# Performance work log

Hardware: AMD Instinct MI355X
Metric: run time of the kernel (lower is better)

Reference implementation:

```python
import jax, jax.numpy as jnp
import numpy as np

HIDDEN = 2048
N_HEADS = 32
N_KV_HEADS = 8
HEAD_DIM = HIDDEN // N_HEADS  # 64
KV_DIM = N_KV_HEADS * HEAD_DIM  # 512


def setup_inputs() -> dict:
    key = jax.random.key(0)
    ks = jax.random.split(key, 9)
    s = 1.0 / np.sqrt(HIDDEN)
    x = jax.random.normal(ks[0], (2, 2048, HIDDEN), dtype=jnp.float32)
    wq = jax.random.uniform(ks[1], (HIDDEN, HIDDEN), jnp.float32, -s, s)
    bq = jax.random.uniform(ks[2], (HIDDEN,), jnp.float32, -s, s)
    wk = jax.random.uniform(ks[3], (KV_DIM, HIDDEN), jnp.float32, -s, s)
    bk = jax.random.uniform(ks[4], (KV_DIM,), jnp.float32, -s, s)
    wv = jax.random.uniform(ks[5], (KV_DIM, HIDDEN), jnp.float32, -s, s)
    bv = jax.random.uniform(ks[6], (KV_DIM,), jnp.float32, -s, s)
    wo = jax.random.uniform(ks[7], (HIDDEN, HIDDEN), jnp.float32, -s, s)
    bo = jax.random.uniform(ks[8], (HIDDEN,), jnp.float32, -s, s)
    return {"x": x, "wq": wq, "bq": bq, "wk": wk, "bk": bk,
            "wv": wv, "bv": bv, "wo": wo, "bo": bo}


def reference(x, wq, bq, wk, bk, wv, bv, wo, bo):
    B, S, _ = x.shape
    group = N_HEADS // N_KV_HEADS  # 4
    # projections (torch Linear: x @ W.T + b)
    q = (x @ wq.T + bq).reshape(B, S, N_HEADS, HEAD_DIM).transpose(0, 2, 1, 3)      # [B,H,S,D]
    k = (x @ wk.T + bk).reshape(B, S, N_KV_HEADS, HEAD_DIM).transpose(0, 2, 1, 3)   # [B,Hk,S,D]
    v = (x @ wv.T + bv).reshape(B, S, N_KV_HEADS, HEAD_DIM).transpose(0, 2, 1, 3)
    # repeat_interleave KV heads to match query heads
    k = jnp.repeat(k, group, axis=1)  # [B,H,S,D]
    v = jnp.repeat(v, group, axis=1)
    scale = 1.0 / np.sqrt(HEAD_DIM).astype(np.float32)
    attn = jnp.einsum('bhqd,bhkd->bhqk', q, k) * scale  # [B,H,S,S]
    score = jax.nn.softmax(attn, axis=-1)
    out = jnp.einsum('bhqk,bhkd->bhqd', score, v)       # [B,H,S,D]
    out = out.transpose(0, 2, 1, 3).reshape(B, S, HIDDEN)
    return out @ wo.T + bo
```

## Files before the change

kernel.cpp:

```cpp
#include <hip/hip_runtime.h>

typedef __attribute__((ext_vector_type(8))) short bf16x8;
typedef __attribute__((ext_vector_type(4))) float f32x4;
typedef __attribute__((ext_vector_type(16))) float f32x16;

__device__ __forceinline__ short f2b(float f) {
  union { unsigned u; float f; } c;
  c.f = f;
  unsigned r = (c.u + 0x7FFFu + ((c.u >> 16) & 1u)) >> 16;
  return (short)r;
}

__device__ __forceinline__ int cvt_pk_bf16(float lo, float hi) {
  int r;
  asm("v_cvt_pk_bf16_f32 %0, %1, %2" : "=v"(r) : "v"(lo), "v"(hi));
  return r;
}

__device__ __forceinline__ void plswap(int& a, int& b) {
  asm volatile("v_permlane32_swap_b32 %0, %1" : "+v"(a), "+v"(b));
}

__device__ __forceinline__ void async16(const void* g, void* l) {
  __builtin_amdgcn_global_load_lds(
      (const __attribute__((address_space(1))) unsigned*)g,
      (__attribute__((address_space(3))) unsigned*)l, 16, 0, 0);
}

__global__ __launch_bounds__(256)
void f32_to_bf16(const float* __restrict__ src, short* __restrict__ dst, int n) {
  int i = (blockIdx.x * blockDim.x + threadIdx.x) * 4;
  if (i < n) {
    float4 v = *(const float4*)(src + i);
    short4 o;
    o.x = f2b(v.x); o.y = f2b(v.y); o.z = f2b(v.z); o.w = f2b(v.w);
    *(short4*)(dst + i) = o;
  }
}

template <bool F32OUT>
__global__ __launch_bounds__(256)
void gemm_bt_bias(const short* __restrict__ A, const short* __restrict__ Bw,
                  const float* __restrict__ bias, void* __restrict__ Cv,
                  int M, int N, int K) {
  __shared__ short lsA[128 * 32];
  __shared__ short lsB[128 * 32];
  const int tid  = threadIdx.x;
  const int wave = tid >> 6, lane = tid & 63;
  const int quad = lane >> 4, lrow = lane & 15;
  const int m0 = blockIdx.y * 128, n0 = blockIdx.x * 128;
  const int wm = (wave >> 1) * 64, wn = (wave & 1) * 64;

  f32x4 zero = {0.f, 0.f, 0.f, 0.f};
  f32x4 acc[4][4];
#pragma unroll
  for (int i = 0; i < 4; i++)
#pragma unroll
    for (int j = 0; j < 4; j++) acc[i][j] = zero;

  const int r0 = tid >> 2, c0 = (tid & 3) * 8;
  const short* Ab  = A  + (size_t)(m0 + r0) * K + c0;
  const short* Ab2 = A  + (size_t)(m0 + r0 + 64) * K + c0;
  const short* Bb  = Bw + (size_t)(n0 + r0) * K + c0;
  const short* Bb2 = Bw + (size_t)(n0 + r0 + 64) * K + c0;

  for (int k0 = 0; k0 < K; k0 += 32) {
    async16(Ab  + k0, lsA + tid * 8);
    async16(Ab2 + k0, lsA + (tid + 256) * 8);
    async16(Bb  + k0, lsB + tid * 8);
    async16(Bb2 + k0, lsB + (tid + 256) * 8);
    __syncthreads();

    bf16x8 af[4], bfr[4];
#pragma unroll
    for (int i = 0; i < 4; i++)
      af[i] = *(const bf16x8*)(lsA + (wm + i * 16 + lrow) * 32 + quad * 8);
#pragma unroll
    for (int j = 0; j < 4; j++)
      bfr[j] = *(const bf16x8*)(lsB + (wn + j * 16 + lrow) * 32 + quad * 8);
#pragma unroll
    for (int i = 0; i < 4; i++)
#pragma unroll
      for (int j = 0; j < 4; j++)
        acc[i][j] = __builtin_amdgcn_mfma_f32_16x16x32_bf16(af[i], bfr[j], acc[i][j], 0, 0, 0);
    __syncthreads();
  }

#pragma unroll
  for (int j = 0; j < 4; j++) {
    const int col = n0 + wn + j * 16 + lrow;
    const float bv = bias[col];
#pragma unroll
    for (int i = 0; i < 4; i++) {
      const int rowb = m0 + wm + i * 16 + quad * 4;
#pragma unroll
      for (int r = 0; r < 4; r++) {
        const float val = acc[i][j][r] + bv;
        if (F32OUT)
          ((float*)Cv)[(size_t)(rowb + r) * N + col] = val;
        else
          ((short*)Cv)[(size_t)(rowb + r) * N + col] = f2b(val);
      }
    }
  }
}

__global__ __launch_bounds__(256)
void gemm_qkv(const short* __restrict__ A, const short* __restrict__ Bw,
              const float* __restrict__ bq, const float* __restrict__ bk,
              const float* __restrict__ bv,
              short* __restrict__ Qo, short* __restrict__ Ko, short* __restrict__ Vo) {
  const int K = 2048;
  __shared__ short lsA[128 * 32];
  __shared__ short lsB[128 * 32];
  const int tid  = threadIdx.x;
  const int wave = tid >> 6, lane = tid & 63;
  const int quad = lane >> 4, lrow = lane & 15;
  const int m0 = blockIdx.y * 128, n0 = blockIdx.x * 128;
  const int wm = (wave >> 1) * 64, wn = (wave & 1) * 64;

  f32x4 zero = {0.f, 0.f, 0.f, 0.f};
  f32x4 acc[4][4];
#pragma unroll
  for (int i = 0; i < 4; i++)
#pragma unroll
    for (int j = 0; j < 4; j++) acc[i][j] = zero;

  const int r0 = tid >> 2, c0 = (tid & 3) * 8;
  const short* Ab  = A  + (size_t)(m0 + r0) * K + c0;
  const short* Ab2 = A  + (size_t)(m0 + r0 + 64) * K + c0;
  const short* Bb  = Bw + (size_t)(n0 + r0) * K + c0;
  const short* Bb2 = Bw + (size_t)(n0 + r0 + 64) * K + c0;

  for (int k0 = 0; k0 < K; k0 += 32) {
    async16(Ab  + k0, lsA + tid * 8);
    async16(Ab2 + k0, lsA + (tid + 256) * 8);
    async16(Bb  + k0, lsB + tid * 8);
    async16(Bb2 + k0, lsB + (tid + 256) * 8);
    __syncthreads();

    bf16x8 af[4], bfr[4];
#pragma unroll
    for (int i = 0; i < 4; i++)
      af[i] = *(const bf16x8*)(lsA + (wm + i * 16 + lrow) * 32 + quad * 8);
#pragma unroll
    for (int j = 0; j < 4; j++)
      bfr[j] = *(const bf16x8*)(lsB + (wn + j * 16 + lrow) * 32 + quad * 8);
#pragma unroll
    for (int i = 0; i < 4; i++)
#pragma unroll
      for (int j = 0; j < 4; j++)
        acc[i][j] = __builtin_amdgcn_mfma_f32_16x16x32_bf16(af[i], bfr[j], acc[i][j], 0, 0, 0);
    __syncthreads();
  }

  short* base; int stride, coff; const float* bias;
  if (n0 < 2048)      { base = Qo; stride = 2048; bias = bq; coff = 0; }
  else if (n0 < 2560) { base = Ko; stride = 512;  bias = bk; coff = 2048; }
  else                { base = Vo; stride = 512;  bias = bv; coff = 2560; }
  const float qs = (n0 < 2048) ? 0.18033688011112043f : 1.0f;

#pragma unroll
  for (int j = 0; j < 4; j++) {
    const int lc = n0 + wn + j * 16 + lrow - coff;
    const float bvv = bias[lc];
#pragma unroll
    for (int i = 0; i < 4; i++) {
      const int rowb = m0 + wm + i * 16 + quad * 4;
#pragma unroll
      for (int r = 0; r < 4; r++)
        base[(size_t)(rowb + r) * stride + lc] = f2b((acc[i][j][r] + bvv) * qs);
    }
  }
}

#define S_LEN 2048
#define HID   2048
#define KVD   512
#define ST    72

__global__ __launch_bounds__(256)
void gqa_flash(const short* __restrict__ Q, const short* __restrict__ Kb,
               const short* __restrict__ Vb, short* __restrict__ O) {
  __shared__ __align__(16) short lsK[64 * ST];
  __shared__ __align__(16) short lsVt[64 * ST];
  __shared__ float lsum[4][32];

  const int tid  = threadIdx.x;
  const int wave = tid >> 6, lane = tid & 63;
  const int l31  = lane & 31, hl = lane >> 5;

  const int d  = blockIdx.x + (blockIdx.y << 6);
  const int by = ((d & 7) << 1) | (d >> 9);
  const int qb = (d >> 3) & 63;
  const int b = by >> 3, kvh = by & 7;
  const int h = kvh * 4 + wave;
  const int q0 = qb * 32;

  const short* Qrow = Q + (size_t)(b * S_LEN + q0 + l31) * HID + h * 64 + hl * 8;
  bf16x8 qf[4];
#pragma unroll
  for (int f = 0; f < 4; f++) qf[f] = *(const bf16x8*)(Qrow + f * 16);

  f32x16 o0, o1;
#pragma unroll
  for (int i = 0; i < 16; i++) { o0[i] = 0.f; o1[i] = 0.f; }
  float lloc = 0.f;

  const short* Kp = Kb + (size_t)b * S_LEN * KVD + kvh * 64;
  const short* Vp = Vb + (size_t)b * S_LEN * KVD + kvh * 64;

  const int keyA = tid >> 3, chK = (tid & 7) * 8;
  const int kpV = tid & 31, dcV = (tid >> 5) * 8;

  bf16x8 kf0 = *(const bf16x8*)(Kp + (size_t)keyA * KVD + chK);
  bf16x8 kf1 = *(const bf16x8*)(Kp + (size_t)(keyA + 32) * KVD + chK);
  bf16x8 vf0 = *(const bf16x8*)(Vp + (size_t)(2 * kpV) * KVD + dcV);
  bf16x8 vf1 = *(const bf16x8*)(Vp + (size_t)(2 * kpV + 1) * KVD + dcV);

  for (int k0 = 0; k0 < S_LEN; k0 += 64) {
    *(bf16x8*)(lsK + keyA * ST + chK) = kf0;
    *(bf16x8*)(lsK + (keyA + 32) * ST + chK) = kf1;
#pragma unroll
    for (int jj = 0; jj < 8; jj++) {
      unsigned pk = (unsigned)(unsigned short)vf0[jj] |
                    ((unsigned)(unsigned short)vf1[jj] << 16);
      *(unsigned*)(lsVt + (dcV + jj) * ST + 2 * kpV) = pk;
    }
    __syncthreads();

    const int kn = (k0 + 64) & (S_LEN - 1);
    kf0 = *(const bf16x8*)(Kp + (size_t)(kn + keyA) * KVD + chK);
    kf1 = *(const bf16x8*)(Kp + (size_t)(kn + keyA + 32) * KVD + chK);
    vf0 = *(const bf16x8*)(Vp + (size_t)(kn + 2 * kpV) * KVD + dcV);
    vf1 = *(const bf16x8*)(Vp + (size_t)(kn + 2 * kpV + 1) * KVD + dcV);

    f32x16 s0, s1;
#pragma unroll
    for (int i = 0; i < 16; i++) { s0[i] = 0.f; s1[i] = 0.f; }
    __builtin_amdgcn_s_setprio(1);
#pragma unroll
    for (int f = 0; f < 4; f++) {
      bf16x8 ka = *(const bf16x8*)(lsK + l31 * ST + f * 16 + hl * 8);
      bf16x8 kb = *(const bf16x8*)(lsK + (32 + l31) * ST + f * 16 + hl * 8);
      s0 = __builtin_amdgcn_mfma_f32_32x32x16_bf16(ka, qf[f], s0, 0, 0, 0);
      s1 = __builtin_amdgcn_mfma_f32_32x32x16_bf16(kb, qf[f], s1, 0, 0, 0);
    }
    __builtin_amdgcn_s_setprio(0);

#pragma unroll
    for (int i = 0; i < 16; i++) {
      s0[i] = __builtin_amdgcn_exp2f(s0[i]);
      s1[i] = __builtin_amdgcn_exp2f(s1[i]);
    }
    {
      f32x16 ps = s0 + s1;
      float a0 = (ps[0] + ps[1]) + (ps[2] + ps[3]);
      float a1 = (ps[4] + ps[5]) + (ps[6] + ps[7]);
      float a2 = (ps[8] + ps[9]) + (ps[10] + ps[11]);
      float a3 = (ps[12] + ps[13]) + (ps[14] + ps[15]);
      lloc += (a0 + a1) + (a2 + a3);
    }
    int P2[2][8];
#pragma unroll
    for (int qq = 0; qq < 8; qq++) {
      P2[0][qq] = cvt_pk_bf16(s0[2 * qq], s0[2 * qq + 1]);
      P2[1][qq] = cvt_pk_bf16(s1[2 * qq], s1[2 * qq + 1]);
    }

    __builtin_amdgcn_s_setprio(1);
#pragma unroll
    for (int t = 0; t < 4; t++) {
      const int j = t >> 1, b0 = (t & 1) * 4;
      int w0 = P2[j][b0 + 0], w2 = P2[j][b0 + 2];
      int w1 = P2[j][b0 + 1], w3 = P2[j][b0 + 3];
      plswap(w0, w2);
      plswap(w1, w3);
      union { unsigned u[4]; bf16x8 v; } pa;
      pa.u[0] = (unsigned)w0; pa.u[1] = (unsigned)w1;
      pa.u[2] = (unsigned)w2; pa.u[3] = (unsigned)w3;
      bf16x8 bv0 = *(const bf16x8*)(lsVt + l31 * ST + t * 16 + hl * 8);
      bf16x8 bv1 = *(const bf16x8*)(lsVt + (32 + l31) * ST + t * 16 + hl * 8);
      o0 = __builtin_amdgcn_mfma_f32_32x32x16_bf16(pa.v, bv0, o0, 0, 0, 0);
      o1 = __builtin_amdgcn_mfma_f32_32x32x16_bf16(pa.v, bv1, o1, 0, 0, 0);
    }
    __builtin_amdgcn_s_setprio(0);
    __syncthreads();
  }

  const float lfull = lloc + __shfl(lloc, lane ^ 32);
  if (lane < 32) lsum[wave][lane] = lfull;
#pragma unroll
  for (int r = 0; r < 16; r++) {
    const int qrow = (r & 3) + 8 * (r >> 2) + 4 * hl;
    const float rl = 1.0f / lsum[wave][qrow];
    short* op = O + (size_t)(b * S_LEN + q0 + qrow) * HID + h * 64 + l31;
    op[0]  = f2b(o0[r] * rl);
    op[32] = f2b(o1[r] * rl);
  }
}

extern "C" void kernel_launch(void* const* d_in, const int* in_sizes, int n_in,
                              void* d_out, int out_size, void* d_ws, size_t ws_size,
                              hipStream_t stream) {
  const float* x  = (const float*)d_in[0];
  const float* wq = (const float*)d_in[1];
  const float* bq = (const float*)d_in[2];
  const float* wk = (const float*)d_in[3];
  const float* bk = (const float*)d_in[4];
  const float* wv = (const float*)d_in[5];
  const float* bv = (const float*)d_in[6];
  const float* wo = (const float*)d_in[7];
  const float* bo = (const float*)d_in[8];
  float* out = (float*)d_out;

  short* xb  = (short*)d_ws;
  short* wqb = xb  + (size_t)4096 * 2048;
  short* wkb = wqb + (size_t)2048 * 2048;
  short* wvb = wkb + (size_t)512 * 2048;
  short* wob = wvb + (size_t)512 * 2048;
  short* Qb  = wob + (size_t)2048 * 2048;
  short* Kb  = Qb  + (size_t)4096 * 2048;
  short* Vb  = Kb  + (size_t)4096 * 512;
  short* AO  = Vb  + (size_t)4096 * 512;

  dim3 blk(256);
  f32_to_bf16<<<4096 * 2048 / 1024, blk, 0, stream>>>(x,  xb,  4096 * 2048);
  f32_to_bf16<<<2048 * 2048 / 1024, blk, 0, stream>>>(wq, wqb, 2048 * 2048);
  f32_to_bf16<<< 512 * 2048 / 1024, blk, 0, stream>>>(wk, wkb, 512 * 2048);
  f32_to_bf16<<< 512 * 2048 / 1024, blk, 0, stream>>>(wv, wvb, 512 * 2048);
  f32_to_bf16<<<2048 * 2048 / 1024, blk, 0, stream>>>(wo, wob, 2048 * 2048);

  gemm_qkv<<<dim3(3072 / 128, 4096 / 128), blk, 0, stream>>>(xb, wqb, bq, bk, bv, Qb, Kb, Vb);
  gqa_flash<<<dim3(2048 / 32, 16), blk, 0, stream>>>(Qb, Kb, Vb, AO);
  gemm_bt_bias<true><<<dim3(2048 / 128, 4096 / 128), blk, 0, stream>>>(AO, wob, bo, out, 4096, 2048, 2048);
}
```

Baseline: 334.6 us.

## Replace projection GEMMs with 256x256 double-buffered pipelined swizzled LDS kernel

Both projection GEMMs (fused QKV and output) now use a single templated kernel with 256x256 tiles, 512 threads, and K-step 64. It double-buffers LDS with async global-to-LDS loads interleaved between MFMA quarter-blocks, and uses XOR-swizzled LDS addressing to avoid bank conflicts. It also remaps workgroup IDs for cache locality and raises MFMA wave priority. The aim is to hide memory latency and raise data reuse per tile. The cost is heavy LDS use (128KB per block) and fewer blocks, which could hurt occupancy or tail behaviour on the smaller output GEMM grid.

```diff
diff --git a/kernel.cpp b/kernel.cpp
--- a/kernel.cpp
+++ b/kernel.cpp
@@ -38,138 +38,184 @@
   }
 }
 
-template <bool F32OUT>
-__global__ __launch_bounds__(256)
-void gemm_bt_bias(const short* __restrict__ A, const short* __restrict__ Bw,
-                  const float* __restrict__ bias, void* __restrict__ Cv,
-                  int M, int N, int K) {
-  __shared__ short lsA[128 * 32];
-  __shared__ short lsB[128 * 32];
+#define GBAR()  do { __builtin_amdgcn_s_barrier(); \
+                     __builtin_amdgcn_sched_barrier(0); } while (0)
+#define WAITV6() do { asm volatile("s_waitcnt vmcnt(6)" ::: "memory"); \
+                      __builtin_amdgcn_sched_barrier(0); } while (0)
+#define WAITV0() do { asm volatile("s_waitcnt vmcnt(0)" ::: "memory"); \
+                      __builtin_amdgcn_sched_barrier(0); } while (0)
+
+template <int MODE>
+__global__ __launch_bounds__(512, 2)
+void gemm256(const short* __restrict__ A, const short* __restrict__ Bw,
+             const float* __restrict__ bq, const float* __restrict__ bk,
+             const float* __restrict__ bv, float* __restrict__ Cf,
+             short* __restrict__ Qo, short* __restrict__ Ko,
+             short* __restrict__ Vo) {
+  constexpr int K  = 2048;
+  constexpr int NT = K / 64;
+  __shared__ short lsA[2][256 * 64];
+  __shared__ short lsB[2][256 * 64];
+
   const int tid  = threadIdx.x;
-  const int wave = tid >> 6, lane = tid & 63;
+  const int lane = tid & 63, wid = tid >> 6;
   const int quad = lane >> 4, lrow = lane & 15;
-  const int m0 = blockIdx.y * 128, n0 = blockIdx.x * 128;
-  const int wm = (wave >> 1) * 64, wn = (wave & 1) * 64;
-
+  const int wr = wid >> 2, wc = wid & 3;
+
+  const int GX  = gridDim.x;
+  const int nwg = GX * gridDim.y;
+  const int dd  = blockIdx.x + blockIdx.y * GX;
+  const int logical = (dd & 7) * (nwg >> 3) + (dd >> 3);
+  const int m0 = (logical / GX) * 256, n0 = (logical % GX) * 256;
+
+  const short* Ab = A  + (size_t)m0 * K;
+  const short* Bb = Bw + (size_t)n0 * K;
+
+  auto stageA = [&](short* lds, int q, int k0) {
+#pragma unroll
+    for (int l = 0; l < 2; l++) {
+      const int L  = l * 512 + tid;
+      const int R  = (((L >> 9) * 2 + q) << 6) + ((L >> 3) & 63);
+      const int cs = L & 7;
+      async16(Ab + (size_t)R * K + k0 + ((cs ^ (R & 7)) << 3),
+              lds + R * 64 + (cs << 3));
+    }
+  };
+  auto stageB = [&](short* lds, int q, int k0) {
+#pragma unroll
+    for (int l = 0; l < 2; l++) {
+      const int L  = l * 512 + tid;
+      const int R  = ((((L >> 8) & 3) * 2 + q) << 5) + ((L >> 3) & 31);
+      const int cs = L & 7;
+      async16(Bb + (size_t)R * K + k0 + ((cs ^ (R & 7)) << 3),
+              lds + R * 64 + (cs << 3));
+    }
+  };
+
+  f32x4 acc[8][4];
   f32x4 zero = {0.f, 0.f, 0.f, 0.f};
-  f32x4 acc[4][4];
-#pragma unroll
-  for (int i = 0; i < 4; i++)
+#pragma unroll
+  for (int i = 0; i < 8; i++)
 #pragma unroll
     for (int j = 0; j < 4; j++) acc[i][j] = zero;
 
-  const int r0 = tid >> 2, c0 = (tid & 3) * 8;
-  const short* Ab  = A  + (size_t)(m0 + r0) * K + c0;
-  const short* Ab2 = A  + (size_t)(m0 + r0 + 64) * K + c0;
-  const short* Bb  = Bw + (size_t)(n0 + r0) * K + c0;
-  const short* Bb2 = Bw + (size_t)(n0 + r0 + 64) * K + c0;
-
-  for (int k0 = 0; k0 < K; k0 += 32) {
-    async16(Ab  + k0, lsA + tid * 8);
-    async16(Ab2 + k0, lsA + (tid + 256) * 8);
-    async16(Bb  + k0, lsB + tid * 8);
-    async16(Bb2 + k0, lsB + (tid + 256) * 8);
-    __syncthreads();
-
-    bf16x8 af[4], bfr[4];
+  bf16x8 a[4][2], b[2][2];
+
+  auto readA = [&](const short* ls, int qr) {
+#pragma unroll
+    for (int i = 0; i < 4; i++) {
+      const int R = wr * 128 + qr * 64 + i * 16 + lrow;
+#pragma unroll
+      for (int kk = 0; kk < 2; kk++)
+        a[i][kk] = *(const bf16x8*)(ls + R * 64 +
+                                    (((kk * 4 + quad) ^ (R & 7)) << 3));
+    }
+  };
+  auto readB = [&](const short* ls, int qc) {
+#pragma unroll
+    for (int j = 0; j < 2; j++) {
+      const int S = wc * 64 + qc * 32 + j * 16 + lrow;
+#pragma unroll
+      for (int kk = 0; kk < 2; kk++)
+        b[j][kk] = *(const bf16x8*)(ls + S * 64 +
+                                    (((kk * 4 + quad) ^ (S & 7)) << 3));
+    }
+  };
+  auto mfma16 = [&](int qr, int qc) {
+    __builtin_amdgcn_s_setprio(1);
 #pragma unroll
     for (int i = 0; i < 4; i++)
-      af[i] = *(const bf16x8*)(lsA + (wm + i * 16 + lrow) * 32 + quad * 8);
-#pragma unroll
-    for (int j = 0; j < 4; j++)
-      bfr[j] = *(const bf16x8*)(lsB + (wn + j * 16 + lrow) * 32 + quad * 8);
-#pragma unroll
-    for (int i = 0; i < 4; i++)
-#pragma unroll
-      for (int j = 0; j < 4; j++)
-        acc[i][j] = __builtin_amdgcn_mfma_f32_16x16x32_bf16(af[i], bfr[j], acc[i][j], 0, 0, 0);
-    __syncthreads();
-  }
-
-#pragma unroll
-  for (int j = 0; j < 4; j++) {
-    const int col = n0 + wn + j * 16 + lrow;
-    const float bv = bias[col];
-#pragma unroll
-    for (int i = 0; i < 4; i++) {
-      const int rowb = m0 + wm + i * 16 + quad * 4;
-#pragma unroll
-      for (int r = 0; r < 4; r++) {
-        const float val = acc[i][j][r] + bv;
-        if (F32OUT)
-          ((float*)Cv)[(size_t)(rowb + r) * N + col] = val;
-        else
-          ((short*)Cv)[(size_t)(rowb + r) * N + col] = f2b(val);
+#pragma unroll
+      for (int j = 0; j < 2; j++) {
+        f32x4 c = acc[qr * 4 + i][qc * 2 + j];
+        c = __builtin_amdgcn_mfma_f32_16x16x32_bf16(a[i][0], b[j][0], c, 0, 0, 0);
+        c = __builtin_amdgcn_mfma_f32_16x16x32_bf16(a[i][1], b[j][1], c, 0, 0, 0);
+        acc[qr * 4 + i][qc * 2 + j] = c;
       }
-    }
-  }
-}
-
-__global__ __launch_bounds__(256)
-void gemm_qkv(const short* __restrict__ A, const short* __restrict__ Bw,
-              const float* __restrict__ bq, const float* __restrict__ bk,
-              const float* __restrict__ bv,
-              short* __restrict__ Qo, short* __restrict__ Ko, short* __restrict__ Vo) {
-  const int K = 2048;
-  __shared__ short lsA[128 * 32];
-  __shared__ short lsB[128 * 32];
-  const int tid  = threadIdx.x;
-  const int wave = tid >> 6, lane = tid & 63;
-  const int quad = lane >> 4, lrow = lane & 15;
-  const int m0 = blockIdx.y * 128, n0 = blockIdx.x * 128;
-  const int wm = (wave >> 1) * 64, wn = (wave & 1) * 64;
-
-  f32x4 zero = {0.f, 0.f, 0.f, 0.f};
-  f32x4 acc[4][4];
-#pragma unroll
-  for (int i = 0; i < 4; i++)
-#pragma unroll
-    for (int j = 0; j < 4; j++) acc[i][j] = zero;
-
-  const int r0 = tid >> 2, c0 = (tid & 3) * 8;
-  const short* Ab  = A  + (size_t)(m0 + r0) * K + c0;
-  const short* Ab2 = A  + (size_t)(m0 + r0 + 64) * K + c0;
-  const short* Bb  = Bw + (size_t)(n0 + r0) * K + c0;
-  const short* Bb2 = Bw + (size_t)(n0 + r0 + 64) * K + c0;
-
-  for (int k0 = 0; k0 < K; k0 += 32) {
-    async16(Ab  + k0, lsA + tid * 8);
-    async16(Ab2 + k0, lsA + (tid + 256) * 8);
-    async16(Bb  + k0, lsB + tid * 8);
-    async16(Bb2 + k0, lsB + (tid + 256) * 8);
-    __syncthreads();
-
-    bf16x8 af[4], bfr[4];
-#pragma unroll
-    for (int i = 0; i < 4; i++)
-      af[i] = *(const bf16x8*)(lsA + (wm + i * 16 + lrow) * 32 + quad * 8);
-#pragma unroll
-    for (int j = 0; j < 4; j++)
-      bfr[j] = *(const bf16x8*)(lsB + (wn + j * 16 + lrow) * 32 + quad * 8);
-#pragma unroll
-    for (int i = 0; i < 4; i++)
-#pragma unroll
-      for (int j = 0; j < 4; j++)
-        acc[i][j] = __builtin_amdgcn_mfma_f32_16x16x32_bf16(af[i], bfr[j], acc[i][j], 0, 0, 0);
-    __syncthreads();
-  }
-
-  short* base; int stride, coff; const float* bias;
-  if (n0 < 2048)      { base = Qo; stride = 2048; bias = bq; coff = 0; }
-  else if (n0 < 2560) { base = Ko; stride = 512;  bias = bk; coff = 2048; }
-  else                { base = Vo; stride = 512;  bias = bv; coff = 2560; }
-  const float qs = (n0 < 2048) ? 0.18033688011112043f : 1.0f;
-
-#pragma unroll
-  for (int j = 0; j < 4; j++) {
-    const int lc = n0 + wn + j * 16 + lrow - coff;
-    const float bvv = bias[lc];
-#pragma unroll
-    for (int i = 0; i < 4; i++) {
-      const int rowb = m0 + wm + i * 16 + quad * 4;
-#pragma unroll
-      for (int r = 0; r < 4; r++)
-        base[(size_t)(rowb + r) * stride + lc] = f2b((acc[i][j][r] + bvv) * qs);
+    __builtin_amdgcn_s_setprio(0);
+  };
+
+  stageA(lsA[0], 0, 0);
+  stageB(lsB[0], 1, 0);
+  stageA(lsA[0], 1, 0);
+  stageB(lsB[0], 0, 0);
+  stageA(lsA[1], 0, 64);
+  stageB(lsB[1], 1, 64);
+  stageA(lsA[1], 1, 64);
+  WAITV6();
+  GBAR();
+
+#pragma unroll 1
+  for (int I = 0; I < NT / 2; I++) {
+    const int u  = 2 * I;
+    const int k1 = (u + 1) * 64;
+    const int k2 = ((u + 2) & (NT - 1)) * 64;
+    const int k3 = ((u + 3) & (NT - 1)) * 64;
+
+    readA(lsA[0], 0); readB(lsB[0], 0);
+    stageB(lsB[1], 0, k1);
+    GBAR(); mfma16(0, 0); GBAR();
+    readB(lsB[0], 1);
+    stageA(lsA[0], 0, k2);
+    GBAR(); mfma16(0, 1); GBAR();
+    readA(lsA[0], 1);
+    stageB(lsB[0], 1, k2);
+    GBAR(); mfma16(1, 1); GBAR();
+    readB(lsB[0], 0);
+    stageA(lsA[0], 1, k2);
+    GBAR(); mfma16(1, 0);
+    WAITV6();
+    GBAR();
+    readA(lsA[1], 0); readB(lsB[1], 0);
+    stageB(lsB[0], 0, k2);
+    GBAR(); mfma16(0, 0); GBAR();
+    readB(lsB[1], 1);
+    stageA(lsA[1], 0, k3);
+    GBAR(); mfma16(0, 1); GBAR();
+    readA(lsA[1], 1);
+    stageB(lsB[1], 1, k3);
+    GBAR(); mfma16(1, 1); GBAR();
+    readB(lsB[1], 0);
+    stageA(lsA[1], 1, k3);
+    GBAR(); mfma16(1, 0);
+    WAITV6();
+    GBAR();
+  }
+
+  WAITV0();
+
+  if (MODE == 0) {
+#pragma unroll
+    for (int j = 0; j < 4; j++) {
+      const int col = n0 + wc * 64 + j * 16 + lrow;
+      const float bb = bq[col];
+#pragma unroll
+      for (int i = 0; i < 8; i++) {
+        const int rowb = m0 + wr * 128 + i * 16 + quad * 4;
+#pragma unroll
+        for (int r = 0; r < 4; r++)
+          Cf[(size_t)(rowb + r) * 2048 + col] = acc[i][j][r] + bb;
+      }
+    }
+  } else {
+    short* base; int stride, coff; const float* bias; float qs;
+    if (n0 < 2048)      { base = Qo; stride = 2048; bias = bq; coff = 0;
+                          qs = 0.18033688011112042f; }
+    else if (n0 < 2560) { base = Ko; stride = 512; bias = bk; coff = 2048;
+                          qs = 1.0f; }
+    else                { base = Vo; stride = 512; bias = bv; coff = 2560;
+                          qs = 1.0f; }
+#pragma unroll
+    for (int j = 0; j < 4; j++) {
+      const int lc = n0 + wc * 64 + j * 16 + lrow - coff;
+      const float bb = bias[lc];
+#pragma unroll
+      for (int i = 0; i < 8; i++) {
+        const int rowb = m0 + wr * 128 + i * 16 + quad * 4;
+#pragma unroll
+        for (int r = 0; r < 4; r++)
+          base[(size_t)(rowb + r) * stride + lc] = f2b((acc[i][j][r] + bb) * qs);
+      }
     }
   }
 }
@@ -331,7 +377,9 @@
   f32_to_bf16<<< 512 * 2048 / 1024, blk, 0, stream>>>(wv, wvb, 512 * 2048);
   f32_to_bf16<<<2048 * 2048 / 1024, blk, 0, stream>>>(wo, wob, 2048 * 2048);
 
-  gemm_qkv<<<dim3(3072 / 128, 4096 / 128), blk, 0, stream>>>(xb, wqb, bq, bk, bv, Qb, Kb, Vb);
+  gemm256<1><<<dim3(3072 / 256, 4096 / 256), dim3(512), 0, stream>>>(
+      xb, wqb, bq, bk, bv, nullptr, Qb, Kb, Vb);
   gqa_flash<<<dim3(2048 / 32, 16), blk, 0, stream>>>(Qb, Kb, Vb, AO);
-  gemm_bt_bias<true><<<dim3(2048 / 128, 4096 / 128), blk, 0, stream>>>(AO, wob, bo, out, 4096, 2048, 2048);
-}
+  gemm256<0><<<dim3(2048 / 256, 4096 / 256), dim3(512), 0, stream>>>(
+      AO, wob, bo, nullptr, nullptr, out, nullptr, nullptr, nullptr);
+}
```

Result: slower. 349.1 us (+4.3%).
